# Performance work log

Hardware: AMD Instinct MI355X
Metric: run time of the kernel (lower is better)

## Reference

```python
import jax, jax.numpy as jnp
import numpy as np

EPS = 1e-5  # torch BatchNorm1d default eps


def _bn_train(h, gamma, beta):
    # BatchNorm1d in training mode over the edge (batch) axes: biased variance.
    m = jnp.mean(h, axis=(0, 1), keepdims=True)
    v = jnp.mean(jnp.square(h - m), axis=(0, 1), keepdims=True)
    return (h - m) * jax.lax.rsqrt(v + EPS) * gamma + beta


def setup_inputs() -> dict:
    key = jax.random.key(0)
    ks = jax.random.split(key, 12)
    N, F, H = 1024, 128, 128
    s1 = 1.0 / np.sqrt(2 * F)
    s2 = 1.0 / np.sqrt(H)
    return {
        "x": jax.random.normal(ks[0], (N, F), dtype=jnp.float32),
        "W1": jax.random.uniform(ks[1], (H, 2 * F), jnp.float32, -s1, s1),
        "b1": jax.random.uniform(ks[2], (H,), jnp.float32, -s1, s1),
        "W2": jax.random.uniform(ks[3], (H, H), jnp.float32, -s2, s2),
        "b2": jax.random.uniform(ks[4], (H,), jnp.float32, -s2, s2),
        "W3": jax.random.uniform(ks[5], (1, H), jnp.float32, -s2, s2),
        "b3": jax.random.uniform(ks[6], (1,), jnp.float32, -s2, s2),
        "g1": jnp.ones((H,), jnp.float32),
        "be1": jnp.zeros((H,), jnp.float32),
        "g2": jnp.ones((H,), jnp.float32),
        "be2": jnp.zeros((H,), jnp.float32),
    }


def reference(x, W1, b1, W2, b2, W3, b3, g1, be1, g2, be2):
    N, F = x.shape
    # Edge e = i*N + j pairs [x[j], x[i]] (row=j varies fast, col=i slow).
    # First Linear on the concat splits into two low-rank GEMMs + broadcast add,
    # avoiding the [N^2, 2F] materialization (same math as Linear(concat)).
    Wa, Wb = W1[:, :F], W1[:, F:]
    A = x @ Wa.T            # contribution of x[row] = x[j] -> varies over axis 1
    B = x @ Wb.T            # contribution of x[col] = x[i] -> varies over axis 0
    h = A[None, :, :] + B[:, None, :] + b1      # [N, N, H], h[i, j]
    h = jax.nn.relu(_bn_train(h, g1, be1))
    h = jnp.einsum('ijh,kh->ijk', h, W2) + b2   # [N, N, H]
    h = jax.nn.relu(_bn_train(h, g2, be2))
    logits = jnp.einsum('ijh,kh->ijk', h, W3)[..., 0] + b3[0]  # [N, N]
    adj = jax.nn.sigmoid((logits + logits.T) * 0.5)
    adj = adj - jnp.diag(jnp.diag(adj))
    return adj
```

## Files before the change

kernel.cpp:

```cpp
#include <hip/hip_runtime.h>
#include <hip/hip_bf16.h>

typedef _Float16 f16x8 __attribute__((ext_vector_type(8)));
typedef _Float16 f16x4 __attribute__((ext_vector_type(4)));
typedef float    f32x4 __attribute__((ext_vector_type(4)));

#define EPSV 1e-5f

__global__ __launch_bounds__(256) void k_ab(const float* __restrict__ x,
                                            const float* __restrict__ W1,
                                            const float* __restrict__ W2,
                                            _Float16* __restrict__ Apf,
                                            _Float16* __restrict__ Btf,
                                            float* __restrict__ gs,
                                            unsigned int* __restrict__ w2p) {
  __shared__ float xs[4 * 128];
  int t = threadIdx.x;
  if (blockIdx.x >= 256) {
    int c = (blockIdx.x - 256) * 256 + t;
    int pair = c & 3;
    int col  = (c >> 2) & 15;
    int quad = (c >> 6) & 3;
    int nt   = (c >> 8) & 7;
    int ks   = (c >> 11) & 3;
    int k = nt * 16 + col;
    int hch = ks * 32 + quad * 8 + pair * 2;
    _Float16 b0 = (_Float16)W2[k * 128 + hch];
    _Float16 b1 = (_Float16)W2[k * 128 + hch + 1];
    unsigned int u0 = *(unsigned short*)&b0, u1 = *(unsigned short*)&b1;
    w2p[c] = u0 | (u1 << 16);
    return;
  }
  int j0 = blockIdx.x * 4;
  for (int idx = t; idx < 512; idx += 256) xs[idx] = x[j0 * 128 + idx];
  __syncthreads();
  int h = t & 127, half = t >> 7;
  const float4* wrow = (const float4*)(W1 + h * 256 + half * 128);
  const float4* xs4 = (const float4*)xs;
  float a0 = 0.f, a1 = 0.f, a2 = 0.f, a3 = 0.f;
#pragma unroll 8
  for (int ch = 0; ch < 32; ++ch) {
    float4 wv = wrow[ch];
    float4 x0 = xs4[ch], x1 = xs4[32 + ch], x2 = xs4[64 + ch], x3 = xs4[96 + ch];
    a0 += wv.x * x0.x + wv.y * x0.y + wv.z * x0.z + wv.w * x0.w;
    a1 += wv.x * x1.x + wv.y * x1.y + wv.z * x1.z + wv.w * x1.w;
    a2 += wv.x * x2.x + wv.y * x2.y + wv.z * x2.z + wv.w * x2.w;
    a3 += wv.x * x3.x + wv.y * x3.y + wv.z * x3.z + wv.w * x3.w;
  }
  if (half == 0) {
    int S = j0 >> 7, s = (j0 >> 4) & 7, colb = j0 & 15;
    int ks = h >> 5, quad = (h >> 3) & 3, eh = (h >> 2) & 1, pos = h & 3;
    int base = S * 16384 + ((s * 4 + ks) * 64 + quad * 16 + colb) * 8 + eh * 4 + pos;
    Apf[base]      = (_Float16)a0;
    Apf[base + 8]  = (_Float16)a1;
    Apf[base + 16] = (_Float16)a2;
    Apf[base + 24] = (_Float16)a3;
  } else {
    Btf[(j0 + 0) * 128 + h] = (_Float16)a0;
    Btf[(j0 + 1) * 128 + h] = (_Float16)a1;
    Btf[(j0 + 2) * 128 + h] = (_Float16)a2;
    Btf[(j0 + 3) * 128 + h] = (_Float16)a3;
  }
  float s = a0 + a1 + a2 + a3;
  float q = a0 * a0 + a1 * a1 + a2 * a2 + a3 * a3;
  atomicAdd(&gs[half * 256 + h], s);
  atomicAdd(&gs[half * 256 + 128 + h], q);
}

__device__ __forceinline__ void f16x8_to_f32(f16x8 v, f32x4& lo, f32x4& hi) {
  f16x4 l4 = __builtin_shufflevector(v, v, 0, 1, 2, 3);
  f16x4 h4 = __builtin_shufflevector(v, v, 4, 5, 6, 7);
  lo = __builtin_convertvector(l4, f32x4);
  hi = __builtin_convertvector(h4, f32x4);
}
__device__ __forceinline__ f16x8 f32_to_f16x8(f32x4 lo, f32x4 hi) {
  f16x4 l4 = __builtin_convertvector(lo, f16x4);
  f16x4 h4 = __builtin_convertvector(hi, f16x4);
  return __builtin_shufflevector(l4, h4, 0, 1, 2, 3, 4, 5, 6, 7);
}

template <int PASS>
__global__ __launch_bounds__(256) void k_pass(
    const _Float16* __restrict__ Apf, const _Float16* __restrict__ Btf,
    const unsigned int* __restrict__ w2p,
    const float* __restrict__ gs, const float* __restrict__ g1,
    const float* __restrict__ be1,
    float* __restrict__ sum2, const float* __restrict__ g2,
    const float* __restrict__ be2, const float* __restrict__ W3v,
    const float* __restrict__ b3p, float* __restrict__ L) {
  __shared__ unsigned int ats[8192];
  __shared__ float red[1024];
  int t = threadIdx.x;
  int bid = blockIdx.x;
  int bj = bid & 7, bi = bid >> 3;
  int lane = t & 63, w = t >> 6;
  int col = lane & 15, quad = lane >> 4;

  const unsigned int* atsrc = (const unsigned int*)Apf + bj * 8192;
#pragma unroll
  for (int it = 0; it < 8; ++it) {
    int g = w * 8 + it;
    __builtin_amdgcn_global_load_lds(
        (const __attribute__((address_space(1))) unsigned int*)(atsrc + g * 256 + lane * 4),
        (__attribute__((address_space(3))) unsigned int*)(ats + g * 256),
        16, 0, 0);
  }

  if (t < 128) {
    const float inv = 1.f / 1024.f;
    float mA = gs[t] * inv;
    float vA = gs[128 + t] * inv - mA * mA;
    float mB = gs[256 + t] * inv;
    float vB = gs[384 + t] * inv - mB * mB;
    float sc = g1[t] * rsqrtf(vA + vB + EPSV);
    red[t] = sc;
    red[128 + t] = be1[t] - mA * sc;
    red[256 + t] = -mB * sc;
  }

  f16x8 bw[4][8];
#pragma unroll
  for (int ks = 0; ks < 4; ++ks)
#pragma unroll
    for (int nt = 0; nt < 8; ++nt)
      bw[ks][nt] = *(const f16x8*)((const _Float16*)w2p + (((ks * 8 + nt) * 64) + lane) * 8);

  float al[8], uu[8], w3l[8];
  float b3v = 0.f;
  if (PASS == 2) {
    b3v = b3p[0];
    const float invM = 1.f / (1024.f * 1024.f);
#pragma unroll
    for (int nt = 0; nt < 8; ++nt) {
      int k = nt * 16 + col;
      float mdot = sum2[k] * invM;
      float var = sum2[128 + k] * invM - mdot * mdot;
      float alv = g2[k] * rsqrtf(var + EPSV);
      al[nt] = alv;
      uu[nt] = be2[k] - mdot * alv;
      w3l[nt] = W3v[k];
    }
  }
  __syncthreads();

  {
    int h0 = ((t >> 6) & 3) * 32 + ((t >> 4) & 3) * 8;
    f32x4 scl = *(const f32x4*)(red + h0);
    f32x4 sch = *(const f32x4*)(red + h0 + 4);
    f32x4 tal = *(const f32x4*)(red + 128 + h0);
    f32x4 tah = *(const f32x4*)(red + 128 + h0 + 4);
#pragma unroll
    for (int k = 0; k < 8; ++k) {
      unsigned int* p = ats + t * 4 + k * 1024;
      f16x8 v = *(f16x8*)p;
      f32x4 lo, hi;
      f16x8_to_f32(v, lo, hi);
      lo = lo * scl + tal;
      hi = hi * sch + tah;
      *(f16x8*)p = f32_to_f16x8(lo, hi);
    }
  }

  f16x8 btr[2][4];
  {
    int i0 = bi * 8 + w * 2;
#pragma unroll
    for (int r = 0; r < 2; ++r)
#pragma unroll
      for (int ks = 0; ks < 4; ++ks) {
        int hh = ks * 32 + quad * 8;
        f16x8 braw = *(const f16x8*)(Btf + (i0 + r) * 128 + hh);
        f32x4 lo, hi;
        f16x8_to_f32(braw, lo, hi);
        f32x4 sl = *(const f32x4*)(red + hh);
        f32x4 sh = *(const f32x4*)(red + hh + 4);
        f32x4 tl = *(const f32x4*)(red + 256 + hh);
        f32x4 th = *(const f32x4*)(red + 256 + hh + 4);
        lo = lo * sl + tl;
        hi = hi * sh + th;
        btr[r][ks] = f32_to_f16x8(lo, hi);
      }
  }
  __syncthreads();

  float s1[8], s2[8];
  if (PASS == 1) {
#pragma unroll
    for (int nt = 0; nt < 8; ++nt) { s1[nt] = 0.f; s2[nt] = 0.f; }
  }

  const f16x8 zz = {(_Float16)0, (_Float16)0, (_Float16)0, (_Float16)0,
                    (_Float16)0, (_Float16)0, (_Float16)0, (_Float16)0};

  for (int s = 0; s < 8; ++s) {
    f32x4 acc[2][8];
#pragma unroll
    for (int mt = 0; mt < 2; ++mt)
#pragma unroll
      for (int nt = 0; nt < 8; ++nt) acc[mt][nt] = (f32x4){0.f, 0.f, 0.f, 0.f};

#pragma unroll
    for (int ks = 0; ks < 4; ++ks) {
      f16x8 af = *(const f16x8*)(ats + ((s * 4 + ks) * 64 + lane) * 4);
      f16x8 a0 = __builtin_elementwise_max(af + btr[0][ks], zz);
      f16x8 a1 = __builtin_elementwise_max(af + btr[1][ks], zz);
#pragma unroll
      for (int nt = 0; nt < 8; ++nt) {
        acc[0][nt] = __builtin_amdgcn_mfma_f32_16x16x32_f16(a0, bw[ks][nt], acc[0][nt], 0, 0, 0);
        acc[1][nt] = __builtin_amdgcn_mfma_f32_16x16x32_f16(a1, bw[ks][nt], acc[1][nt], 0, 0, 0);
      }
    }

    if (PASS == 1) {
#pragma unroll
      for (int nt = 0; nt < 8; ++nt)
#pragma unroll
        for (int mt = 0; mt < 2; ++mt)
#pragma unroll
          for (int r = 0; r < 4; ++r) {
            float d = acc[mt][nt][r];
            s1[nt] += d;
            s2[nt] = fmaf(d, d, s2[nt]);
          }
    } else {
#pragma unroll
      for (int mt = 0; mt < 2; ++mt) {
        float rsum[4] = {0.f, 0.f, 0.f, 0.f};
#pragma unroll
        for (int nt = 0; nt < 8; ++nt)
#pragma unroll
          for (int r = 0; r < 4; ++r) {
            float h = fmaxf(fmaf(acc[mt][nt][r], al[nt], uu[nt]), 0.f);
            rsum[r] = fmaf(h, w3l[nt], rsum[r]);
          }
#pragma unroll
        for (int r = 0; r < 4; ++r) {
          rsum[r] += __shfl_xor(rsum[r], 1);
          rsum[r] += __shfl_xor(rsum[r], 2);
          rsum[r] += __shfl_xor(rsum[r], 4);
          rsum[r] += __shfl_xor(rsum[r], 8);
        }
        if (col == 0) {
          int i = bi * 8 + w * 2 + mt;
          float4 v = make_float4(rsum[0] + b3v, rsum[1] + b3v,
                                 rsum[2] + b3v, rsum[3] + b3v);
          *(float4*)(&L[i * 1024 + bj * 128 + s * 16 + quad * 4]) = v;
        }
      }
    }
  }

  if (PASS == 1) {
#pragma unroll
    for (int nt = 0; nt < 8; ++nt) {
      s1[nt] += __shfl_xor(s1[nt], 16);
      s1[nt] += __shfl_xor(s1[nt], 32);
      s2[nt] += __shfl_xor(s2[nt], 16);
      s2[nt] += __shfl_xor(s2[nt], 32);
    }
    __syncthreads();
    if (lane < 16) {
#pragma unroll
      for (int nt = 0; nt < 8; ++nt) {
        red[w * 256 + nt * 16 + lane] = s1[nt];
        red[w * 256 + 128 + nt * 16 + lane] = s2[nt];
      }
    }
    __syncthreads();
    float tot = red[t] + red[256 + t] + red[512 + t] + red[768 + t];
    atomicAdd(&sum2[t], tot);
  }
}

__global__ __launch_bounds__(256) void k_adj(const float* __restrict__ L,
                                             float* __restrict__ out) {
  int idx = blockIdx.x * 256 + threadIdx.x;
  int i = idx >> 10, j = idx & 1023;
  float a = L[i * 1024 + j];
  float b = L[j * 1024 + i];
  float s = 1.f / (1.f + __expf(-0.5f * (a + b)));
  out[idx] = (i == j) ? 0.f : s;
}

extern "C" void kernel_launch(void* const* d_in, const int* in_sizes, int n_in,
                              void* d_out, int out_size, void* d_ws, size_t ws_size,
                              hipStream_t stream) {
  const float* x   = (const float*)d_in[0];
  const float* W1  = (const float*)d_in[1];
  const float* W2  = (const float*)d_in[3];
  const float* W3  = (const float*)d_in[5];
  const float* b3  = (const float*)d_in[6];
  const float* g1  = (const float*)d_in[7];
  const float* be1 = (const float*)d_in[8];
  const float* g2  = (const float*)d_in[9];
  const float* be2 = (const float*)d_in[10];

  float* ws = (float*)d_ws;
  _Float16* Apf     = (_Float16*)ws;
  _Float16* Btf     = (_Float16*)(ws + 65536);
  unsigned int* w2p = (unsigned int*)(ws + 131072);
  float* gs         = ws + 139264;
  float* sum2       = ws + 139776;
  float* L          = ws + 140032;
  float* out        = (float*)d_out;

  hipMemsetAsync(gs, 0, 768 * sizeof(float), stream);

  k_ab<<<288, 256, 0, stream>>>(x, W1, W2, Apf, Btf, gs, w2p);
  k_pass<1><<<1024, 256, 0, stream>>>(Apf, Btf, w2p, gs, g1, be1, sum2,
                                      nullptr, nullptr, nullptr, nullptr, nullptr);
  k_pass<2><<<1024, 256, 0, stream>>>(Apf, Btf, w2p, gs, g1, be1, sum2,
                                      g2, be2, W3, b3, L);
  k_adj<<<4096, 256, 0, stream>>>(L, out);
}
```

Baseline: 207.4 us.

## Split output channels across wave pairs to halve per-wave W2 register footprint

Each wave now computes only half of the 128 output channels of the second linear layer (4 of 8 N-tiles), so the B-operand registers for W2 shrink by half. It instead iterates over 4 rows of i instead of 2. The normalized B rows are staged once in shared memory rather than held in registers. Partial logits from the two channel halves are combined through a shared-memory buffer before the global store, and the BN2 statistics reduction is remapped to match. The intent is lower VGPR pressure and higher occupancy, at the cost of extra LDS traffic and another barrier.

```diff
diff --git a/kernel.cpp b/kernel.cpp
--- a/kernel.cpp
+++ b/kernel.cpp
@@ -90,10 +90,13 @@
     const float* __restrict__ b3p, float* __restrict__ L) {
   __shared__ unsigned int ats[8192];
   __shared__ float red[1024];
+  __shared__ unsigned int btl[512];
+  __shared__ float P[2048];
   int t = threadIdx.x;
   int bid = blockIdx.x;
   int bj = bid & 7, bi = bid >> 3;
   int lane = t & 63, w = t >> 6;
+  int ig = w >> 1, kg = w & 1;
   int col = lane & 15, quad = lane >> 4;
 
   const unsigned int* atsrc = (const unsigned int*)Apf + bj * 8192;
@@ -118,21 +121,22 @@
     red[256 + t] = -mB * sc;
   }
 
-  f16x8 bw[4][8];
+  f16x8 bw[4][4];
 #pragma unroll
   for (int ks = 0; ks < 4; ++ks)
 #pragma unroll
-    for (int nt = 0; nt < 8; ++nt)
-      bw[ks][nt] = *(const f16x8*)((const _Float16*)w2p + (((ks * 8 + nt) * 64) + lane) * 8);
-
-  float al[8], uu[8], w3l[8];
+    for (int nt = 0; nt < 4; ++nt)
+      bw[ks][nt] = *(const f16x8*)((const _Float16*)w2p +
+                                   (((ks * 8 + kg * 4 + nt) * 64) + lane) * 8);
+
+  float al[4], uu[4], w3l[4];
   float b3v = 0.f;
   if (PASS == 2) {
     b3v = b3p[0];
     const float invM = 1.f / (1024.f * 1024.f);
 #pragma unroll
-    for (int nt = 0; nt < 8; ++nt) {
-      int k = nt * 16 + col;
+    for (int nt = 0; nt < 4; ++nt) {
+      int k = (kg * 4 + nt) * 16 + col;
       float mdot = sum2[k] * invM;
       float var = sum2[128 + k] * invM - mdot * mdot;
       float alv = g2[k] * rsqrtf(var + EPSV);
@@ -161,76 +165,66 @@
     }
   }
 
-  f16x8 btr[2][4];
-  {
-    int i0 = bi * 8 + w * 2;
-#pragma unroll
-    for (int r = 0; r < 2; ++r)
-#pragma unroll
-      for (int ks = 0; ks < 4; ++ks) {
-        int hh = ks * 32 + quad * 8;
-        f16x8 braw = *(const f16x8*)(Btf + (i0 + r) * 128 + hh);
-        f32x4 lo, hi;
-        f16x8_to_f32(braw, lo, hi);
-        f32x4 sl = *(const f32x4*)(red + hh);
-        f32x4 sh = *(const f32x4*)(red + hh + 4);
-        f32x4 tl = *(const f32x4*)(red + 256 + hh);
-        f32x4 th = *(const f32x4*)(red + 256 + hh + 4);
-        lo = lo * sl + tl;
-        hi = hi * sh + th;
-        btr[r][ks] = f32_to_f16x8(lo, hi);
-      }
+  if (t < 128) {
+    int r = t >> 4, c8 = (t & 15) * 8;
+    f16x8 braw = *(const f16x8*)(Btf + (bi * 8 + r) * 128 + c8);
+    f32x4 lo, hi;
+    f16x8_to_f32(braw, lo, hi);
+    f32x4 sl = *(const f32x4*)(red + c8);
+    f32x4 sh = *(const f32x4*)(red + c8 + 4);
+    f32x4 tl = *(const f32x4*)(red + 256 + c8);
+    f32x4 th = *(const f32x4*)(red + 256 + c8 + 4);
+    lo = lo * sl + tl;
+    hi = hi * sh + th;
+    *(f16x8*)((_Float16*)btl + r * 128 + c8) = f32_to_f16x8(lo, hi);
   }
   __syncthreads();
 
-  float s1[8], s2[8];
+  float s1[4], s2[4];
   if (PASS == 1) {
 #pragma unroll
-    for (int nt = 0; nt < 8; ++nt) { s1[nt] = 0.f; s2[nt] = 0.f; }
+    for (int nt = 0; nt < 4; ++nt) { s1[nt] = 0.f; s2[nt] = 0.f; }
   }
 
   const f16x8 zz = {(_Float16)0, (_Float16)0, (_Float16)0, (_Float16)0,
                     (_Float16)0, (_Float16)0, (_Float16)0, (_Float16)0};
 
-  for (int s = 0; s < 8; ++s) {
-    f32x4 acc[2][8];
-#pragma unroll
-    for (int mt = 0; mt < 2; ++mt)
-#pragma unroll
-      for (int nt = 0; nt < 8; ++nt) acc[mt][nt] = (f32x4){0.f, 0.f, 0.f, 0.f};
-
-#pragma unroll
-    for (int ks = 0; ks < 4; ++ks) {
-      f16x8 af = *(const f16x8*)(ats + ((s * 4 + ks) * 64 + lane) * 4);
-      f16x8 a0 = __builtin_elementwise_max(af + btr[0][ks], zz);
-      f16x8 a1 = __builtin_elementwise_max(af + btr[1][ks], zz);
-#pragma unroll
-      for (int nt = 0; nt < 8; ++nt) {
-        acc[0][nt] = __builtin_amdgcn_mfma_f32_16x16x32_f16(a0, bw[ks][nt], acc[0][nt], 0, 0, 0);
-        acc[1][nt] = __builtin_amdgcn_mfma_f32_16x16x32_f16(a1, bw[ks][nt], acc[1][nt], 0, 0, 0);
+  for (int il = 0; il < 4; ++il) {
+    f16x8 btr[4];
+#pragma unroll
+    for (int ks = 0; ks < 4; ++ks)
+      btr[ks] = *(const f16x8*)((const _Float16*)btl + (ig * 4 + il) * 128 + ks * 32 + quad * 8);
+
+    for (int s = 0; s < 8; ++s) {
+      f32x4 acc[4];
+#pragma unroll
+      for (int nt = 0; nt < 4; ++nt) acc[nt] = (f32x4){0.f, 0.f, 0.f, 0.f};
+
+#pragma unroll
+      for (int ks = 0; ks < 4; ++ks) {
+        f16x8 af = *(const f16x8*)(ats + ((s * 4 + ks) * 64 + lane) * 4);
+        f16x8 a = __builtin_elementwise_max(af + btr[ks], zz);
+#pragma unroll
+        for (int nt = 0; nt < 4; ++nt)
+          acc[nt] = __builtin_amdgcn_mfma_f32_16x16x32_f16(a, bw[ks][nt], acc[nt], 0, 0, 0);
       }
-    }
-
-    if (PASS == 1) {
-#pragma unroll
-      for (int nt = 0; nt < 8; ++nt)
-#pragma unroll
-        for (int mt = 0; mt < 2; ++mt)
+
+      if (PASS == 1) {
+#pragma unroll
+        for (int nt = 0; nt < 4; ++nt)
 #pragma unroll
           for (int r = 0; r < 4; ++r) {
-            float d = acc[mt][nt][r];
+            float d = acc[nt][r];
             s1[nt] += d;
             s2[nt] = fmaf(d, d, s2[nt]);
           }
-    } else {
-#pragma unroll
-      for (int mt = 0; mt < 2; ++mt) {
+      } else {
         float rsum[4] = {0.f, 0.f, 0.f, 0.f};
 #pragma unroll
-        for (int nt = 0; nt < 8; ++nt)
+        for (int nt = 0; nt < 4; ++nt)
 #pragma unroll
           for (int r = 0; r < 4; ++r) {
-            float h = fmaxf(fmaf(acc[mt][nt][r], al[nt], uu[nt]), 0.f);
+            float h = fmaxf(fmaf(acc[nt][r], al[nt], uu[nt]), 0.f);
             rsum[r] = fmaf(h, w3l[nt], rsum[r]);
           }
 #pragma unroll
@@ -241,10 +235,9 @@
           rsum[r] += __shfl_xor(rsum[r], 8);
         }
         if (col == 0) {
-          int i = bi * 8 + w * 2 + mt;
-          float4 v = make_float4(rsum[0] + b3v, rsum[1] + b3v,
-                                 rsum[2] + b3v, rsum[3] + b3v);
-          *(float4*)(&L[i * 1024 + bj * 128 + s * 16 + quad * 4]) = v;
+          int slot = kg * 1024 + (ig * 4 + il) * 128 + s * 16 + quad * 4;
+#pragma unroll
+          for (int r = 0; r < 4; ++r) P[slot + r] = rsum[r];
         }
       }
     }
@@ -252,7 +245,7 @@
 
   if (PASS == 1) {
 #pragma unroll
-    for (int nt = 0; nt < 8; ++nt) {
+    for (int nt = 0; nt < 4; ++nt) {
       s1[nt] += __shfl_xor(s1[nt], 16);
       s1[nt] += __shfl_xor(s1[nt], 32);
       s2[nt] += __shfl_xor(s2[nt], 16);
@@ -261,14 +254,30 @@
     __syncthreads();
     if (lane < 16) {
 #pragma unroll
-      for (int nt = 0; nt < 8; ++nt) {
-        red[w * 256 + nt * 16 + lane] = s1[nt];
-        red[w * 256 + 128 + nt * 16 + lane] = s2[nt];
+      for (int nt = 0; nt < 4; ++nt) {
+        red[w * 128 + nt * 16 + lane] = s1[nt];
+        red[w * 128 + 64 + nt * 16 + lane] = s2[nt];
       }
     }
     __syncthreads();
-    float tot = red[t] + red[256 + t] + red[512 + t] + red[768 + t];
-    atomicAdd(&sum2[t], tot);
+    {
+      int k = t & 127;
+      int kgc = k >> 6;
+      int loc = k & 63;
+      int off = (t >> 7) * 64;
+      float v = red[kgc * 128 + off + loc] + red[(2 + kgc) * 128 + off + loc];
+      atomicAdd(&sum2[(t >> 7) * 128 + k], v);
+    }
+  } else {
+    __syncthreads();
+#pragma unroll
+    for (int rep = 0; rep < 4; ++rep) {
+      int slot = rep * 256 + t;
+      float v = P[slot] + P[1024 + slot] + b3v;
+      int i = bi * 8 + (slot >> 7);
+      int j = bj * 128 + (slot & 127);
+      L[i * 1024 + j] = v;
+    }
   }
 }
 
```

Result: faster. 196.1 us (-5.4%).
